# Kernel tuning notes

Hardware: AMD Instinct MI355X
Metric: run time of the kernel (lower is better)

The kernel has to match this reference:

```python
import jax, jax.numpy as jnp
import numpy as np

N_NODES = 100000
N_EDGES = 3200000
IN_FEAT = 512
HIDDEN = 64
N_GRAPHS = 2048


def setup_inputs() -> dict:
    key = jax.random.key(0)
    ks = jax.random.split(key, 8)
    x = jax.random.normal(ks[0], (N_NODES, IN_FEAT), dtype=jnp.float32)
    edge_index = jax.random.randint(ks[1], (2, N_EDGES), 0, N_NODES, dtype=jnp.int64)
    batch = jnp.sort(jax.random.randint(ks[2], (N_NODES,), 0, N_GRAPHS, dtype=jnp.int64))
    W1 = jax.random.normal(ks[3], (IN_FEAT, HIDDEN), dtype=jnp.float32) * (1.0 / np.sqrt(IN_FEAT))
    b1 = jnp.zeros((HIDDEN,), dtype=jnp.float32)
    W2 = jax.random.normal(ks[4], (HIDDEN, HIDDEN), dtype=jnp.float32) * (1.0 / np.sqrt(HIDDEN))
    b2 = jnp.zeros((HIDDEN,), dtype=jnp.float32)
    fc_w = jax.random.normal(ks[5], (HIDDEN, 1), dtype=jnp.float32) * (1.0 / np.sqrt(HIDDEN))
    fc_b = jnp.zeros((1,), dtype=jnp.float32)
    return {"x": x, "edge_index": edge_index, "batch": batch, "num_graphs": N_GRAPHS,
            "W1": W1, "b1": b1, "W2": W2, "b2": b2, "fc_w": fc_w, "fc_b": fc_b}


def _gcn_conv(x, src, dst, n_nodes, W, b):
    # PyG GCNConv: h = X W; out = D^{-1/2}(A+I)D^{-1/2} h + b  (self-loops already in src/dst)
    h = x @ W  # [N, out]
    ones = jnp.ones_like(src, dtype=h.dtype)
    deg = jax.ops.segment_sum(ones, dst, num_segments=n_nodes)  # in-degree incl. self-loop
    dinv = jnp.where(deg > 0, jax.lax.rsqrt(deg), 0.0)
    norm = dinv[src] * dinv[dst]  # [E+N]
    msgs = h[src] * norm[:, None]  # gather + scale
    out = jax.ops.segment_sum(msgs, dst, num_segments=n_nodes)  # scatter-add
    return out + b


def reference(x, edge_index, batch, num_graphs, W1, b1, W2, b2, fc_w, fc_b):
    n = x.shape[0]
    loops = jnp.arange(n, dtype=edge_index.dtype)
    src = jnp.concatenate([edge_index[0], loops])
    dst = jnp.concatenate([edge_index[1], loops])

    h = jax.nn.relu(_gcn_conv(x, src, dst, n, W1, b1))
    h = _gcn_conv(h, src, dst, n, W2, b2)

    # global_mean_pool over graph ids
    sums = jax.ops.segment_sum(h, batch, num_segments=num_graphs)
    cnts = jax.ops.segment_sum(jnp.ones((n,), dtype=h.dtype), batch, num_segments=num_graphs)
    pooled = sums / jnp.maximum(cnts, 1.0)[:, None]
    return pooled @ fc_w + fc_b  # [num_graphs, 1]
```

## Files before the change

### kernel.cpp

```cpp
#include <hip/hip_runtime.h>
#include <hip/hip_bf16.h>

#define N_NODES  100000
#define N_EDGES  3200000
#define IN_FEAT  512
#define HIDDEN   64
#define N_GRAPHS 2048
#define CAP      96

typedef __attribute__((ext_vector_type(8))) short short8;
typedef __attribute__((ext_vector_type(4))) float floatx4;

__device__ inline void bf16_split(float f, short& hi, short& lo) {
    unsigned u = __float_as_uint(f);
    unsigned r = (u + 0x7fffu + ((u >> 16) & 1u)) >> 16;
    float fh = __uint_as_float(r << 16);
    float fl = f - fh;
    unsigned v = __float_as_uint(fl);
    unsigned s = (v + 0x7fffu + ((v >> 16) & 1u)) >> 16;
    hi = (short)r;
    lo = (short)s;
}

__global__ __launch_bounds__(256) void fused_init(float* __restrict__ pooled,
                                                  int* __restrict__ degi,
                                                  int* __restrict__ cntg,
                                                  const int* __restrict__ batch,
                                                  int n, int g) {
    int i = blockIdx.x * 256 + threadIdx.x;
    if (i < g * 64) pooled[i] = 0.f;
    if (i < n) degi[i] = 1;
    if (i < g) {
        int lo0 = 0, hi0 = n;
        while (lo0 < hi0) { int m = (lo0 + hi0) >> 1; if (batch[m] < i) lo0 = m + 1; else hi0 = m; }
        int lo1 = lo0, hi1 = n;
        while (lo1 < hi1) { int m = (lo1 + hi1) >> 1; if (batch[m] < i + 1) lo1 = m + 1; else hi1 = m; }
        cntg[i] = lo1 - lo0;
    }
}

__global__ __launch_bounds__(256) void split_w(const float* __restrict__ W,
                                               short* __restrict__ hi_t,
                                               short* __restrict__ lo_t, int K) {
    int i = blockIdx.x * 256 + threadIdx.x;
    if (i < K * 64) {
        int k = i >> 6, c = i & 63;
        short h, l;
        bf16_split(W[i], h, l);
        hi_t[c * K + k] = h;
        lo_t[c * K + k] = l;
    }
}

__global__ __launch_bounds__(256) void deg_scatter(const int* __restrict__ src,
                                                   const int* __restrict__ dst,
                                                   int* __restrict__ degi,
                                                   int* __restrict__ csr_pad, int e) {
    int i = (blockIdx.x * 256 + threadIdx.x) * 4;
    if (i + 4 <= e) {
        int4 d = *(const int4*)(dst + i);
        int4 s = *(const int4*)(src + i);
        int r;
        r = atomicAdd(&degi[d.x], 1) - 1; if (r < CAP) csr_pad[d.x * CAP + r] = s.x;
        r = atomicAdd(&degi[d.y], 1) - 1; if (r < CAP) csr_pad[d.y * CAP + r] = s.y;
        r = atomicAdd(&degi[d.z], 1) - 1; if (r < CAP) csr_pad[d.z * CAP + r] = s.z;
        r = atomicAdd(&degi[d.w], 1) - 1; if (r < CAP) csr_pad[d.w * CAP + r] = s.w;
    } else {
        for (int j = i; j < e; j++) {
            int r = atomicAdd(&degi[dst[j]], 1) - 1;
            if (r < CAP) csr_pad[dst[j] * CAP + r] = src[j];
        }
    }
}

template <int K>
__global__ __launch_bounds__(256) void gemm_mfma(const float* __restrict__ X,
                                                 const short* __restrict__ Whi,
                                                 const short* __restrict__ Wlo,
                                                 const int* __restrict__ degi,
                                                 float* __restrict__ Y, int nrows) {
    constexpr int BSTR = 40;
    __shared__ short bhi[64 * BSTR];
    __shared__ short blo[64 * BSTR];

    const int t    = threadIdx.x;
    const int wave = t >> 6;
    const int lane = t & 63;
    const int quad = lane >> 4;
    const int l16  = lane & 15;

    const int arow   = blockIdx.x * 64 + wave * 16 + l16;
    const bool rvalid = arow < nrows;
    const float* xrow = X + (size_t)arow * K;

    const int scol = t & 63;
    const int skg  = t >> 6;
    const short* whp = Whi + (size_t)scol * K + skg * 8;
    const short* wlp = Wlo + (size_t)scol * K + skg * 8;

    floatx4 acc[4] = {};

#pragma unroll 1
    for (int k0 = 0; k0 < K; k0 += 32) {
        short8 whi = *(const short8*)(whp + k0);
        short8 wlo = *(const short8*)(wlp + k0);

        float av[8] = {0.f, 0.f, 0.f, 0.f, 0.f, 0.f, 0.f, 0.f};
        if (rvalid) {
            float4 p0 = *(const float4*)(xrow + k0 + quad * 8);
            float4 p1 = *(const float4*)(xrow + k0 + quad * 8 + 4);
            av[0] = p0.x; av[1] = p0.y; av[2] = p0.z; av[3] = p0.w;
            av[4] = p1.x; av[5] = p1.y; av[6] = p1.z; av[7] = p1.w;
        }
        short8 ahi, alo;
#pragma unroll
        for (int j = 0; j < 8; j++) { short h, l; bf16_split(av[j], h, l); ahi[j] = h; alo[j] = l; }

        __syncthreads();
        *(short8*)&bhi[scol * BSTR + skg * 8] = whi;
        *(short8*)&blo[scol * BSTR + skg * 8] = wlo;
        __syncthreads();

#pragma unroll
        for (int ct = 0; ct < 4; ct++) {
            int col = ct * 16 + l16;
            short8 bh = *(short8*)&bhi[col * BSTR + quad * 8];
            short8 bl = *(short8*)&blo[col * BSTR + quad * 8];
            acc[ct] = __builtin_amdgcn_mfma_f32_16x16x32_bf16(ahi, bh, acc[ct], 0, 0, 0);
            acc[ct] = __builtin_amdgcn_mfma_f32_16x16x32_bf16(ahi, bl, acc[ct], 0, 0, 0);
            acc[ct] = __builtin_amdgcn_mfma_f32_16x16x32_bf16(alo, bh, acc[ct], 0, 0, 0);
        }
    }

#pragma unroll
    for (int r = 0; r < 4; r++) {
        int orow = blockIdx.x * 64 + wave * 16 + quad * 4 + r;
        if (orow < nrows) {
            float dv = 1.0f / sqrtf((float)degi[orow]);
#pragma unroll
            for (int ct = 0; ct < 4; ct++)
                Y[(size_t)orow * 64 + ct * 16 + l16] = acc[ct][r] * dv;
        }
    }
}

template <bool RELU, bool POOL>
__global__ __launch_bounds__(256) void gcn_gather(const float* __restrict__ g,
                                                  const int* __restrict__ degi,
                                                  const int* __restrict__ csr_pad,
                                                  const float* __restrict__ bias,
                                                  float* __restrict__ out,
                                                  float* __restrict__ pooled,
                                                  const int* __restrict__ batch, int n) {
    int node = (blockIdx.x * 256 + threadIdx.x) >> 6;
    int lane = threadIdx.x & 63;
    int es = lane >> 4;
    int fg = lane & 15;
    if (node >= n) return;

    int dg = degi[node];
    int de = min(dg - 1, CAP);
    float dn = 1.0f / sqrtf((float)dg);
    int start = node * CAP;

    float4 a0 = make_float4(0.f, 0.f, 0.f, 0.f);
    float4 a1 = a0, a2 = a0, a3 = a0;
    if (es == 0) a0 = *(const float4*)(g + (size_t)node * 64 + fg * 4);

    for (int c = 0; c < de; c += 64) {
        int m = min(64, de - c);
        int sv = (lane < m) ? csr_pad[start + c + lane] : -1;
        int t = 0;
        for (; t + 16 <= m; t += 16) {
            int s0 = __shfl(sv, t + es);
            int s1 = __shfl(sv, t + 4 + es);
            int s2 = __shfl(sv, t + 8 + es);
            int s3 = __shfl(sv, t + 12 + es);
            float4 v0 = *(const float4*)(g + (size_t)s0 * 64 + fg * 4);
            float4 v1 = *(const float4*)(g + (size_t)s1 * 64 + fg * 4);
            float4 v2 = *(const float4*)(g + (size_t)s2 * 64 + fg * 4);
            float4 v3 = *(const float4*)(g + (size_t)s3 * 64 + fg * 4);
            a0.x += v0.x; a0.y += v0.y; a0.z += v0.z; a0.w += v0.w;
            a1.x += v1.x; a1.y += v1.y; a1.z += v1.z; a1.w += v1.w;
            a2.x += v2.x; a2.y += v2.y; a2.z += v2.z; a2.w += v2.w;
            a3.x += v3.x; a3.y += v3.y; a3.z += v3.z; a3.w += v3.w;
        }
        for (; t < m; t += 4) {
            int e = t + es;
            int s = __shfl(sv, e);
            if (e < m) {
                float4 v = *(const float4*)(g + (size_t)s * 64 + fg * 4);
                a0.x += v.x; a0.y += v.y; a0.z += v.z; a0.w += v.w;
            }
        }
    }
    float4 a;
    a.x = (a0.x + a1.x) + (a2.x + a3.x);
    a.y = (a0.y + a1.y) + (a2.y + a3.y);
    a.z = (a0.z + a1.z) + (a2.z + a3.z);
    a.w = (a0.w + a1.w) + (a2.w + a3.w);
    a.x += __shfl_xor(a.x, 16); a.y += __shfl_xor(a.y, 16);
    a.z += __shfl_xor(a.z, 16); a.w += __shfl_xor(a.w, 16);
    a.x += __shfl_xor(a.x, 32); a.y += __shfl_xor(a.y, 32);
    a.z += __shfl_xor(a.z, 32); a.w += __shfl_xor(a.w, 32);

    if (es == 0) {
        float4 bv = *(const float4*)(bias + fg * 4);
        float4 o;
        o.x = fmaf(dn, a.x, bv.x);
        o.y = fmaf(dn, a.y, bv.y);
        o.z = fmaf(dn, a.z, bv.z);
        o.w = fmaf(dn, a.w, bv.w);
        if (RELU) {
            o.x = fmaxf(o.x, 0.f); o.y = fmaxf(o.y, 0.f);
            o.z = fmaxf(o.z, 0.f); o.w = fmaxf(o.w, 0.f);
        }
        if (POOL) {
            float* pp = pooled + (size_t)batch[node] * 64 + fg * 4;
            atomicAdd(pp + 0, o.x);
            atomicAdd(pp + 1, o.y);
            atomicAdd(pp + 2, o.z);
            atomicAdd(pp + 3, o.w);
        } else {
            *(float4*)(out + (size_t)node * 64 + fg * 4) = o;
        }
    }
}

__global__ __launch_bounds__(256) void final_fc(const float* __restrict__ pooled,
                                                const int* __restrict__ cntg,
                                                const float* __restrict__ fc_w,
                                                const float* __restrict__ fc_b,
                                                float* __restrict__ out, int g) {
    int gid = (blockIdx.x * 256 + threadIdx.x) >> 6;
    int lane = threadIdx.x & 63;
    if (gid >= g) return;
    float c = fmaxf((float)cntg[gid], 1.0f);
    float v = pooled[(size_t)gid * 64 + lane] / c * fc_w[lane];
#pragma unroll
    for (int off = 32; off > 0; off >>= 1) v += __shfl_down(v, off);
    if (lane == 0) out[gid] = v + fc_b[0];
}

extern "C" void kernel_launch(void* const* d_in, const int* in_sizes, int n_in,
                              void* d_out, int out_size, void* d_ws, size_t ws_size,
                              hipStream_t stream) {
    const float* x    = (const float*)d_in[0];
    const int*   eidx = (const int*)d_in[1];
    const int*   batch= (const int*)d_in[2];
    const float* W1   = (const float*)d_in[4];
    const float* b1   = (const float*)d_in[5];
    const float* W2   = (const float*)d_in[6];
    const float* b2   = (const float*)d_in[7];
    const float* fc_w = (const float*)d_in[8];
    const float* fc_b = (const float*)d_in[9];
    float* out = (float*)d_out;

    const int N = in_sizes[0] / IN_FEAT;
    const int E = in_sizes[1] / 2;
    const int G = N_GRAPHS;
    const int* src = eidx;
    const int* dst = eidx + E;

    char* w = (char*)d_ws;
    float* g1   = (float*)w; w += (size_t)N * 64 * 4;
    float* h1r  = (float*)w; w += (size_t)N * 64 * 4;
    float* g2   = (float*)w; w += (size_t)N * 64 * 4;
    int*   degi = (int*)w;   w += (size_t)N * 4;
    int*   csrp = (int*)w;   w += (size_t)N * CAP * 4;
    float* pooled = (float*)w; w += (size_t)G * 64 * 4;
    int*   cntg = (int*)w;   w += (size_t)G * 4;
    short* w1hi = (short*)w; w += (size_t)IN_FEAT * 64 * 2;
    short* w1lo = (short*)w; w += (size_t)IN_FEAT * 64 * 2;
    short* w2hi = (short*)w; w += (size_t)HIDDEN * 64 * 2;
    short* w2lo = (short*)w; w += (size_t)HIDDEN * 64 * 2;

    fused_init<<<(G * 64 + 255) / 256, 256, 0, stream>>>(pooled, degi, cntg, batch, N, G);
    split_w<<<(IN_FEAT * 64 + 255) / 256, 256, 0, stream>>>(W1, w1hi, w1lo, IN_FEAT);
    split_w<<<(HIDDEN * 64 + 255) / 256, 256, 0, stream>>>(W2, w2hi, w2lo, HIDDEN);
    deg_scatter<<<(E / 4 + 255) / 256, 256, 0, stream>>>(src, dst, degi, csrp, E);

    gemm_mfma<IN_FEAT><<<(N + 63) / 64, 256, 0, stream>>>(x, w1hi, w1lo, degi, g1, N);
    gcn_gather<true, false><<<(N * 64 + 255) / 256, 256, 0, stream>>>(
        g1, degi, csrp, b1, h1r, nullptr, batch, N);
    gemm_mfma<HIDDEN><<<(N + 63) / 64, 256, 0, stream>>>(h1r, w2hi, w2lo, degi, g2, N);
    gcn_gather<false, true><<<(N * 64 + 255) / 256, 256, 0, stream>>>(
        g2, degi, csrp, b2, nullptr, pooled, batch, N);
    final_fc<<<(G * 64 + 255) / 256, 256, 0, stream>>>(pooled, cntg, fc_w, fc_b, out, G);
}
```

Baseline: 873.1 us.

## Build exact CSR via two-level bucket sort instead of padded atomic scatter

Result: faster. 743.0 us (-14.9%).

```diff
diff --git a/kernel.cpp b/kernel.cpp
--- a/kernel.cpp
+++ b/kernel.cpp
@@ -6,7 +6,11 @@
 #define IN_FEAT  512
 #define HIDDEN   64
 #define N_GRAPHS 2048
-#define CAP      96
+#define BSH      8
+#define NPB      256
+#define NBK      512
+#define BCAP     10240
+#define CH       4096
 
 typedef __attribute__((ext_vector_type(8))) short short8;
 typedef __attribute__((ext_vector_type(4))) float floatx4;
@@ -23,13 +27,13 @@
 }
 
 __global__ __launch_bounds__(256) void fused_init(float* __restrict__ pooled,
-                                                  int* __restrict__ degi,
                                                   int* __restrict__ cntg,
+                                                  int* __restrict__ bcnt,
                                                   const int* __restrict__ batch,
                                                   int n, int g) {
     int i = blockIdx.x * 256 + threadIdx.x;
     if (i < g * 64) pooled[i] = 0.f;
-    if (i < n) degi[i] = 1;
+    if (i < NBK) bcnt[i] = 0;
     if (i < g) {
         int lo0 = 0, hi0 = n;
         while (lo0 < hi0) { int m = (lo0 + hi0) >> 1; if (batch[m] < i) lo0 = m + 1; else hi0 = m; }
@@ -52,24 +56,111 @@
     }
 }
 
-__global__ __launch_bounds__(256) void deg_scatter(const int* __restrict__ src,
-                                                   const int* __restrict__ dst,
-                                                   int* __restrict__ degi,
-                                                   int* __restrict__ csr_pad, int e) {
-    int i = (blockIdx.x * 256 + threadIdx.x) * 4;
-    if (i + 4 <= e) {
-        int4 d = *(const int4*)(dst + i);
-        int4 s = *(const int4*)(src + i);
-        int r;
-        r = atomicAdd(&degi[d.x], 1) - 1; if (r < CAP) csr_pad[d.x * CAP + r] = s.x;
-        r = atomicAdd(&degi[d.y], 1) - 1; if (r < CAP) csr_pad[d.y * CAP + r] = s.y;
-        r = atomicAdd(&degi[d.z], 1) - 1; if (r < CAP) csr_pad[d.z * CAP + r] = s.z;
-        r = atomicAdd(&degi[d.w], 1) - 1; if (r < CAP) csr_pad[d.w * CAP + r] = s.w;
-    } else {
-        for (int j = i; j < e; j++) {
-            int r = atomicAdd(&degi[dst[j]], 1) - 1;
-            if (r < CAP) csr_pad[dst[j] * CAP + r] = src[j];
-        }
+__global__ __launch_bounds__(256) void bucket_count(const int* __restrict__ dst,
+                                                    int* __restrict__ bcnt, int e) {
+    __shared__ int lcnt[NBK];
+    for (int b = threadIdx.x; b < NBK; b += 256) lcnt[b] = 0;
+    __syncthreads();
+    int i = blockIdx.x * 256 + threadIdx.x;
+    int stride = gridDim.x * 256;
+    for (; i < e; i += stride) atomicAdd(&lcnt[dst[i] >> BSH], 1);
+    __syncthreads();
+    for (int b = threadIdx.x; b < NBK; b += 256) {
+        int c = lcnt[b];
+        if (c) atomicAdd(&bcnt[b], c);
+    }
+}
+
+__global__ void bucket_scan(const int* __restrict__ bcnt,
+                            int* __restrict__ boff,
+                            int* __restrict__ tail, int nb) {
+    __shared__ int sA[512], sB[512];
+    int t = threadIdx.x;
+    int v = (t < nb) ? bcnt[t] : 0;
+    sA[t] = v;
+    __syncthreads();
+    int* pin = sA; int* pout = sB;
+    for (int off = 1; off < 512; off <<= 1) {
+        pout[t] = pin[t] + ((t >= off) ? pin[t - off] : 0);
+        __syncthreads();
+        int* tmp = pin; pin = pout; pout = tmp;
+    }
+    if (t < nb) { boff[t] = pin[t] - v; tail[t] = pin[t] - v; }
+    if (t == 0) boff[nb] = pin[nb - 1];
+}
+
+__global__ __launch_bounds__(256) void bucket_scatter(const int* __restrict__ src,
+                                                      const int* __restrict__ dst,
+                                                      int* __restrict__ tail,
+                                                      unsigned* __restrict__ packed, int e) {
+    __shared__ int lcnt[NBK];
+    __shared__ int sbase[NBK];
+    int t = threadIdx.x;
+    for (int b = t; b < NBK; b += 256) lcnt[b] = 0;
+    __syncthreads();
+    int base = blockIdx.x * CH;
+    int bk[16]; int rk[16]; unsigned pk[16];
+#pragma unroll
+    for (int j = 0; j < 16; j++) {
+        int idx = base + j * 256 + t;
+        bk[j] = -1;
+        if (idx < e) {
+            int d = dst[idx], s = src[idx];
+            bk[j] = d >> BSH;
+            pk[j] = ((unsigned)(d & (NPB - 1)) << 17) | (unsigned)s;
+            rk[j] = atomicAdd(&lcnt[bk[j]], 1);
+        }
+    }
+    __syncthreads();
+    for (int b = t; b < NBK; b += 256) {
+        int c = lcnt[b];
+        sbase[b] = c ? atomicAdd(&tail[b], c) : 0;
+    }
+    __syncthreads();
+#pragma unroll
+    for (int j = 0; j < 16; j++)
+        if (bk[j] >= 0) packed[sbase[bk[j]] + rk[j]] = pk[j];
+}
+
+__global__ __launch_bounds__(256) void bucket_csr(const unsigned* __restrict__ packed,
+                                                  const int* __restrict__ boff,
+                                                  int* __restrict__ csr,
+                                                  int* __restrict__ row_start,
+                                                  int* __restrict__ degi, int n) {
+    __shared__ unsigned ed[BCAP];
+    __shared__ int deg[NPB], excl[NPB], sA[NPB], sB[NPB];
+    int b = blockIdx.x, t = threadIdx.x;
+    int gbase = boff[b];
+    int cnt = boff[b + 1] - gbase;
+    if (cnt > BCAP) cnt = BCAP;
+    for (int i = t; i < cnt; i += 256) ed[i] = packed[gbase + i];
+    deg[t] = 0;
+    __syncthreads();
+    for (int i = t; i < cnt; i += 256) atomicAdd(&deg[ed[i] >> 17], 1);
+    __syncthreads();
+    sA[t] = deg[t];
+    __syncthreads();
+    int* pin = sA; int* pout = sB;
+    for (int off = 1; off < NPB; off <<= 1) {
+        pout[t] = pin[t] + ((t >= off) ? pin[t - off] : 0);
+        __syncthreads();
+        int* tmp = pin; pin = pout; pout = tmp;
+    }
+    excl[t] = pin[t] - deg[t];
+    __syncthreads();
+    int n0 = b << BSH;
+    if (n0 + t < n) {
+        row_start[n0 + t] = gbase + excl[t];
+        degi[n0 + t] = deg[t] + 1;
+    }
+    __syncthreads();
+    deg[t] = excl[t];
+    __syncthreads();
+    for (int i = t; i < cnt; i += 256) {
+        unsigned p = ed[i];
+        int d = p >> 17;
+        int slot = atomicAdd(&deg[d], 1);
+        csr[gbase + slot] = (int)(p & 0x1FFFFu);
     }
 }
 
@@ -147,7 +238,8 @@
 template <bool RELU, bool POOL>
 __global__ __launch_bounds__(256) void gcn_gather(const float* __restrict__ g,
                                                   const int* __restrict__ degi,
-                                                  const int* __restrict__ csr_pad,
+                                                  const int* __restrict__ row_start,
+                                                  const int* __restrict__ csr_src,
                                                   const float* __restrict__ bias,
                                                   float* __restrict__ out,
                                                   float* __restrict__ pooled,
@@ -159,9 +251,9 @@
     if (node >= n) return;
 
     int dg = degi[node];
-    int de = min(dg - 1, CAP);
+    int de = dg - 1;
     float dn = 1.0f / sqrtf((float)dg);
-    int start = node * CAP;
+    int start = row_start[node];
 
     float4 a0 = make_float4(0.f, 0.f, 0.f, 0.f);
     float4 a1 = a0, a2 = a0, a3 = a0;
@@ -169,7 +261,7 @@
 
     for (int c = 0; c < de; c += 64) {
         int m = min(64, de - c);
-        int sv = (lane < m) ? csr_pad[start + c + lane] : -1;
+        int sv = (lane < m) ? csr_src[start + c + lane] : -1;
         int t = 0;
         for (; t + 16 <= m; t += 16) {
             int s0 = __shfl(sv, t + es);
@@ -261,13 +353,19 @@
     const int G = N_GRAPHS;
     const int* src = eidx;
     const int* dst = eidx + E;
+    const int nb = (N + NPB - 1) >> BSH;
 
     char* w = (char*)d_ws;
     float* g1   = (float*)w; w += (size_t)N * 64 * 4;
     float* h1r  = (float*)w; w += (size_t)N * 64 * 4;
     float* g2   = (float*)w; w += (size_t)N * 64 * 4;
     int*   degi = (int*)w;   w += (size_t)N * 4;
-    int*   csrp = (int*)w;   w += (size_t)N * CAP * 4;
+    int*   rowst= (int*)w;   w += (size_t)N * 4;
+    int*   bcnt = (int*)w;   w += NBK * 4;
+    int*   boff = (int*)w;   w += (NBK + 1) * 4 + 12;
+    int*   tail = (int*)w;   w += NBK * 4;
+    unsigned* packed = (unsigned*)w; w += (size_t)E * 4;
+    int*   csrs = (int*)w;   w += (size_t)E * 4;
     float* pooled = (float*)w; w += (size_t)G * 64 * 4;
     int*   cntg = (int*)w;   w += (size_t)G * 4;
     short* w1hi = (short*)w; w += (size_t)IN_FEAT * 64 * 2;
@@ -275,16 +373,20 @@
     short* w2hi = (short*)w; w += (size_t)HIDDEN * 64 * 2;
     short* w2lo = (short*)w; w += (size_t)HIDDEN * 64 * 2;
 
-    fused_init<<<(G * 64 + 255) / 256, 256, 0, stream>>>(pooled, degi, cntg, batch, N, G);
+    fused_init<<<(G * 64 + 255) / 256, 256, 0, stream>>>(pooled, cntg, bcnt, batch, N, G);
     split_w<<<(IN_FEAT * 64 + 255) / 256, 256, 0, stream>>>(W1, w1hi, w1lo, IN_FEAT);
     split_w<<<(HIDDEN * 64 + 255) / 256, 256, 0, stream>>>(W2, w2hi, w2lo, HIDDEN);
-    deg_scatter<<<(E / 4 + 255) / 256, 256, 0, stream>>>(src, dst, degi, csrp, E);
+
+    bucket_count<<<2048, 256, 0, stream>>>(dst, bcnt, E);
+    bucket_scan<<<1, 512, 0, stream>>>(bcnt, boff, tail, nb);
+    bucket_scatter<<<(E + CH - 1) / CH, 256, 0, stream>>>(src, dst, tail, packed, E);
+    bucket_csr<<<nb, 256, 0, stream>>>(packed, boff, csrs, rowst, degi, N);
 
     gemm_mfma<IN_FEAT><<<(N + 63) / 64, 256, 0, stream>>>(x, w1hi, w1lo, degi, g1, N);
     gcn_gather<true, false><<<(N * 64 + 255) / 256, 256, 0, stream>>>(
-        g1, degi, csrp, b1, h1r, nullptr, batch, N);
+        g1, degi, rowst, csrs, b1, h1r, nullptr, batch, N);
     gemm_mfma<HIDDEN><<<(N + 63) / 64, 256, 0, stream>>>(h1r, w2hi, w2lo, degi, g2, N);
     gcn_gather<false, true><<<(N * 64 + 255) / 256, 256, 0, stream>>>(
-        g2, degi, csrp, b2, nullptr, pooled, batch, N);
+        g2, degi, rowst, csrs, b2, nullptr, pooled, batch, N);
     final_fc<<<(G * 64 + 255) / 256, 256, 0, stream>>>(pooled, cntg, fc_w, fc_b, out, G);
 }
```
